# Kernel optimization log

Hardware: AMD Instinct MI355X
Metric: run time of the kernel (lower is better)

The kernel has to match this reference:

```python
import jax, jax.numpy as jnp
import numpy as np

T, N, F, H = 64, 20000, 8, 32
E = 320000
NEG_SLOPE = 0.01  # torch.nn.LeakyReLU default


def setup_inputs() -> dict:
    key = jax.random.key(0)
    ks = jax.random.split(key, 16)
    g = lambda k, shape, fan_in: jax.random.normal(k, shape, jnp.float32) * (1.0 / np.sqrt(fan_in))
    return {
        "x": jax.random.normal(ks[0], (T, N, F), jnp.float32),
        "edge_index": jax.random.randint(ks[1], (2, E), 0, N, jnp.int64),
        "edge_weight": jax.random.uniform(ks[2], (E,), jnp.float32),
        "h": jnp.zeros((N, H), jnp.float32),
        # GConvGRU(K=1): each ChebConv reduces to a dense Linear (only T_0 = X term)
        "Wxz": g(ks[3], (F, H), F), "bxz": jnp.zeros((H,), jnp.float32),
        "Whz": g(ks[4], (H, H), H), "bhz": jnp.zeros((H,), jnp.float32),
        "Wxr": g(ks[5], (F, H), F), "bxr": jnp.zeros((H,), jnp.float32),
        "Whr": g(ks[6], (H, H), H), "bhr": jnp.zeros((H,), jnp.float32),
        "Wxh": g(ks[7], (F, H), F), "bxh": jnp.zeros((H,), jnp.float32),
        "Whh": g(ks[8], (H, H), H), "bhh": jnp.zeros((H,), jnp.float32),
        "W1": g(ks[9], (H, 1), H), "b1": jnp.zeros((1,), jnp.float32),
        "W2": g(ks[10], (N, 1), N), "b2": jnp.zeros((1,), jnp.float32),
    }


def reference(x, edge_index, edge_weight, h,
              Wxz, bxz, Whz, bhz, Wxr, bxr, Whr, bhr, Wxh, bxh, Whh, bhh,
              W1, b1, W2, b2):
    # GConvGRU with Chebyshev order K=1: each ChebConv is out = X @ W + b
    # (edge_index / edge_weight only participate for K >= 2, faithful to source).
    def gru_step(hc, xt):  # hc: [N,H], xt: [N,F]
        z = jax.nn.sigmoid(xt @ Wxz + bxz + hc @ Whz + bhz)
        r = jax.nn.sigmoid(xt @ Wxr + bxr + hc @ Whr + bhr)
        h_tilde = jnp.tanh(xt @ Wxh + bxh + (hc * r) @ Whh + bhh)
        hn = z * hc + (1.0 - z) * h_tilde
        return hn, hn

    h_fin, h_tensor = jax.lax.scan(gru_step, h, x)  # h_tensor: [T,N,H]
    a = jax.nn.leaky_relu(h_tensor, NEG_SLOPE)       # LeakyReLU(h_tensor)
    a = jax.nn.leaky_relu(a @ W1 + b1, NEG_SLOPE)    # linear1 -> [T,N,1], then LeakyReLU
    a = a[..., 0]                                    # squeeze -> [T,N]
    out = (a @ W2 + b2)[..., 0]                      # linear2 -> [T,1] -> squeeze -> [T]
    return (out, h_fin)
```

## Files before the change

### kernel.cpp

```cpp
#include <hip/hip_runtime.h>
#include <hip/hip_bf16.h>

#define T_STEPS 64
#define N_NODES 20000
#define F_IN    8
#define H_DIM   32
#define NEG_SLOPE 0.01f
#define WS_STRIDE 32
#define LOG2E 1.44269504f

typedef __attribute__((ext_vector_type(8))) short bf16x8;
typedef __attribute__((ext_vector_type(4))) float f32x4;

#define MFMA(a, b, c) __builtin_amdgcn_mfma_f32_16x16x32_bf16((a), (b), (c), 0, 0, 0)

__device__ __forceinline__ unsigned short f2bf(float f) {
    unsigned u = __float_as_uint(f);
    u += 0x7FFFu + ((u >> 16) & 1u);
    return (unsigned short)(u >> 16);
}
__device__ __forceinline__ float bf2f(unsigned short s) {
    return __uint_as_float(((unsigned)s) << 16);
}
__device__ __forceinline__ void split_pack8_rne(const float* v, bf16x8& hi, bf16x8& lo) {
    union { unsigned u[4]; bf16x8 v8; } H, L;
#pragma unroll
    for (int p = 0; p < 4; ++p) {
        float a = v[2*p], b = v[2*p+1];
        unsigned short ha = f2bf(a), hb = f2bf(b);
        unsigned short la = f2bf(a - bf2f(ha)), lb = f2bf(b - bf2f(hb));
        H.u[p] = (unsigned)ha | ((unsigned)hb << 16);
        L.u[p] = (unsigned)la | ((unsigned)lb << 16);
    }
    hi = H.v8; lo = L.v8;
}

__device__ __forceinline__ unsigned cvtpk(float a, float b) {
    union { __hip_bfloat162 h; unsigned u; } U;
    U.h = __float22bfloat162_rn(float2{a, b});
    return U.u;
}


__device__ __forceinline__ void load_wfragW(const float* __restrict__ W, int c, int q,
                                            int Rout, int Rown, int Roth, float scale,
                                            bf16x8& hi, bf16x8& lo) {
    float v[8];
#pragma unroll
    for (int j = 0; j < 8; ++j) {
        int dim = (j < 4) ? (Rown + 4*q + j) : (Roth + 4*q + (j - 4));
        v[j] = W[dim * H_DIM + (Rout + c)] * scale;
    }
    split_pack8_rne(v, hi, lo);
}

__device__ __forceinline__ bf16x8 load_xwfragW(const float* __restrict__ Wx,
                                               const float* __restrict__ bx,
                                               const float* __restrict__ bh,
                                               int c, int q, int Rout, float scale) {
    union { unsigned short s[8]; bf16x8 v8; } U;
#pragma unroll
    for (int j = 0; j < 8; ++j) U.s[j] = 0;
    if (q == 0) {
#pragma unroll
        for (int j = 0; j < 8; ++j) U.s[j] = f2bf(Wx[j * H_DIM + Rout + c] * scale);
    } else if (q == 1) {
#pragma unroll
        for (int j = 0; j < 8; ++j) {
            float w0 = Wx[j * H_DIM + Rout + c] * scale;
            unsigned short h = f2bf(w0);
            U.s[j] = f2bf(w0 - bf2f(h));
        }
    } else if (q == 3) {
        float b = (bx[Rout + c] + bh[Rout + c]) * scale;
        unsigned short h = f2bf(b);
        U.s[0] = h;
        U.s[1] = f2bf(b - bf2f(h));
    }
    return U.v8;
}

__device__ __forceinline__ bf16x8 frag4(unsigned o01, unsigned o23,
                                        unsigned p01, unsigned p23) {
    union { unsigned u[4]; bf16x8 v8; } U;
    U.u[0] = o01; U.u[1] = o23; U.u[2] = p01; U.u[3] = p23;
    return U.v8;
}

__device__ __forceinline__ float sigmoid2_f(float xp) {
    return __builtin_amdgcn_rcpf(1.0f + __builtin_amdgcn_exp2f(-xp));
}
__device__ __forceinline__ float tanh2_f(float yp) {
    return 1.0f - 2.0f * __builtin_amdgcn_rcpf(1.0f + __builtin_amdgcn_exp2f(yp));
}
__device__ __forceinline__ float leaky_f(float x) {
    return fmaxf(x, NEG_SLOPE * x);
}

__global__ void final_kernel(const float* __restrict__ ws, const float* __restrict__ b2,
                             float* __restrict__ out) {
    int t = threadIdx.x;
    if (t < T_STEPS) out[t] = ws[t * WS_STRIDE] + b2[0];
}

__global__ __launch_bounds__(128, 3) void rgcn_mfma_kernel(
    const float* __restrict__ x,
    const float* __restrict__ h0,
    const float* __restrict__ Wxz, const float* __restrict__ bxz,
    const float* __restrict__ Whz, const float* __restrict__ bhz,
    const float* __restrict__ Wxr, const float* __restrict__ bxr,
    const float* __restrict__ Whr, const float* __restrict__ bhr,
    const float* __restrict__ Wxh, const float* __restrict__ bxh,
    const float* __restrict__ Whh, const float* __restrict__ bhh,
    const float* __restrict__ W1,  const float* __restrict__ b1,
    const float* __restrict__ W2,
    float* __restrict__ ws,
    float* __restrict__ out)
{
    const int tid  = threadIdx.x;
    const int w    = tid >> 6;
    const int l    = tid & 63;
    const int c    = l & 15;
    const int q    = l >> 4;
    const int base = blockIdx.x * 16;
    const int node = base + c;
    const int Rown = 16 * w;
    const int Roth = 16 - Rown;

    __shared__ __align__(16) unsigned xbuf[T_STEPS][16][4];
    __shared__ __align__(8) uint2 hxbuf[2][2][4][16];
    __shared__ __align__(8) uint2 rhbuf[2][4][16];
    __shared__ unsigned short pbuf16[T_STEPS][2][17];

    bf16x8 WHrh, WHrl, WHzh, WHzl, WHhh, WHhl;
    load_wfragW(Whr, c, q, Rown, Rown, Roth, LOG2E,        WHrh, WHrl);
    load_wfragW(Whz, c, q, Rown, Rown, Roth, LOG2E,        WHzh, WHzl);
    load_wfragW(Whh, c, q, Rown, Rown, Roth, 2.0f * LOG2E, WHhh, WHhl);
    bf16x8 WXr = load_xwfragW(Wxr, bxr, bhr, c, q, Rown, LOG2E);
    bf16x8 WXz = load_xwfragW(Wxz, bxz, bhz, c, q, Rown, LOG2E);
    bf16x8 WXh = load_xwfragW(Wxh, bxh, bhh, c, q, Rown, 2.0f * LOG2E);

    float w1v[4];
#pragma unroll
    for (int i = 0; i < 4; ++i) w1v[i] = W1[Rown + 4*q + i];
    const float b1s = b1[0];
    const float w2l = W2[node];

    float hv[4];
    unsigned own01, own23;
    {
        float4 h4 = ((const float4*)(h0 + (size_t)node * H_DIM + Rown))[q];
        hv[0] = h4.x; hv[1] = h4.y; hv[2] = h4.z; hv[3] = h4.w;
        own01 = cvtpk(hv[0], hv[1]);
        own23 = cvtpk(hv[2], hv[3]);
        hxbuf[0][w][q][c] = uint2{own01, own23};
    }

#pragma unroll
    for (int it = 0; it < 16; ++it) {
        int idx = it * 128 + tid;
        int t   = idx >> 5;
        int ce  = (idx >> 1) & 15;
        int hf  = idx & 1;
        const float4 v = *(const float4*)(
            x + ((size_t)t * N_NODES + base + ce) * F_IN + hf * 4);
        xbuf[t][ce][hf * 2]     = cvtpk(v.x, v.y);
        xbuf[t][ce][hf * 2 + 1] = cvtpk(v.z, v.w);
    }

    const f32x4 zero4 = {0.0f, 0.0f, 0.0f, 0.0f};
    const unsigned ONES2 = 0x3F803F80u;
    const bool q3 = (q == 3);

    __syncthreads();

    f32x4 axr, axz, axh;
    {
        union { uint4 u4; } X; X.u4 = *(const uint4*)&xbuf[0][c][0];
        bf16x8 fx0 = frag4(q3 ? ONES2 : X.u4.x, X.u4.y, X.u4.z, X.u4.w);
        axr = MFMA(WXr, fx0, zero4);
        axz = MFMA(WXz, fx0, zero4);
        axh = MFMA(WXh, fx0, zero4);
    }

#pragma unroll 1
    for (int t = 0; t < T_STEPS; ++t) {
        const int rp = t & 1;

        uint2 ohp = hxbuf[rp][1 - w][q][c];
        bf16x8 fh = frag4(own01, own23, ohp.x, ohp.y);

        f32x4 arA = MFMA(WHrh, fh, axr);
        f32x4 arB = MFMA(WHrl, fh, zero4);
        f32x4 az  = MFMA(WHzh, fh, axz);
        az        = MFMA(WHzl, fh, az);
        f32x4 ar  = arA + arB;

        float rh4[4];
#pragma unroll
        for (int i = 0; i < 4; ++i) rh4[i] = sigmoid2_f(ar[i]) * hv[i];
        unsigned rh01 = cvtpk(rh4[0], rh4[1]);
        unsigned rh23 = cvtpk(rh4[2], rh4[3]);
        rhbuf[w][q][c] = uint2{rh01, rh23};

        __syncthreads();

        int tt = (t + 1 < T_STEPS) ? (t + 1) : (T_STEPS - 1);
        union { uint4 u4; } X; X.u4 = *(const uint4*)&xbuf[tt][c][0];
        uint2 orh = rhbuf[1 - w][q][c];

        bf16x8 fxn = frag4(q3 ? ONES2 : X.u4.x, X.u4.y, X.u4.z, X.u4.w);
        f32x4 nxr = MFMA(WXr, fxn, zero4);
        f32x4 nxz = MFMA(WXz, fxn, zero4);
        f32x4 nxh = MFMA(WXh, fxn, zero4);

        float zv[4];
#pragma unroll
        for (int i = 0; i < 4; ++i) zv[i] = sigmoid2_f(az[i]);

        bf16x8 fr = frag4(rh01, rh23, orh.x, orh.y);
        f32x4 ahA = MFMA(WHhh, fr, axh);
        f32x4 ahB = MFMA(WHhl, fr, zero4);
        f32x4 ah  = ahA + ahB;

        float pnew = 0.0f;
#pragma unroll
        for (int i = 0; i < 4; ++i) {
            float th = tanh2_f(ah[i]);
            float hn = th + zv[i] * (hv[i] - th);
            hv[i] = hn;
            pnew = fmaf(leaky_f(hn), w1v[i], pnew);
        }
        pnew += __shfl_xor(pnew, 16);
        pnew += __shfl_xor(pnew, 32);
        if (l < 16) pbuf16[t][w][c] = (unsigned short)cvtpk(pnew, pnew);

        own01 = cvtpk(hv[0], hv[1]);
        own23 = cvtpk(hv[2], hv[3]);
        hxbuf[1 - rp][w][q][c] = uint2{own01, own23};

        axr = nxr; axz = nxz; axh = nxh;

        __syncthreads();
    }

#pragma unroll
    for (int rep = 0; rep < 8; ++rep) {
        int t = w * 32 + rep * 4 + q;
        float s = bf2f(pbuf16[t][0][c]) + bf2f(pbuf16[t][1][c]);
        float a2 = leaky_f(s + b1s) * w2l;
        a2 += __shfl_xor(a2, 1); a2 += __shfl_xor(a2, 2);
        a2 += __shfl_xor(a2, 4); a2 += __shfl_xor(a2, 8);
        if (c == 0) atomicAdd(&ws[t * WS_STRIDE], a2);
    }

    *(float4*)(out + T_STEPS + (size_t)node * H_DIM + Rown + 4*q) =
        (float4){hv[0], hv[1], hv[2], hv[3]};
}

extern "C" void kernel_launch(void* const* d_in, const int* in_sizes, int n_in,
                              void* d_out, int out_size, void* d_ws, size_t ws_size,
                              hipStream_t stream) {
    const float* x    = (const float*)d_in[0];
    const float* h0   = (const float*)d_in[3];
    const float* Wxz  = (const float*)d_in[4];
    const float* bxz  = (const float*)d_in[5];
    const float* Whz  = (const float*)d_in[6];
    const float* bhz  = (const float*)d_in[7];
    const float* Wxr  = (const float*)d_in[8];
    const float* bxr  = (const float*)d_in[9];
    const float* Whr  = (const float*)d_in[10];
    const float* bhr  = (const float*)d_in[11];
    const float* Wxh  = (const float*)d_in[12];
    const float* bxh  = (const float*)d_in[13];
    const float* Whh  = (const float*)d_in[14];
    const float* bhh  = (const float*)d_in[15];
    const float* W1   = (const float*)d_in[16];
    const float* b1   = (const float*)d_in[17];
    const float* W2   = (const float*)d_in[18];
    const float* b2   = (const float*)d_in[19];
    float* out = (float*)d_out;
    float* ws  = (float*)d_ws;

    const int grid = N_NODES / 16;
    rgcn_mfma_kernel<<<grid, 128, 0, stream>>>(
        x, h0, Wxz, bxz, Whz, bhz, Wxr, bxr, Whr, bhr,
        Wxh, bxh, Whh, bhh, W1, b1, W2, ws, out);

    final_kernel<<<1, 64, 0, stream>>>(ws, b2, out);
}
```

Measured before the change: 179.2 us.

## Compute reset gate redundantly for both halves to drop mid-step barrier

Each wave now also computes the reset gate for the other wave's half of the hidden state, using the other half's previous h already read from shared memory. It builds the full r*h fragment locally, so the rhbuf shared-memory exchange and one __syncthreads per timestep go away. In exchange each wave issues three extra MFMAs per step (two for the other half's Whr, one for its Wxr) and keeps more weight fragments in registers. The next-step x load is also hoisted to the top of the loop.

```diff
diff --git a/kernel.cpp b/kernel.cpp
--- a/kernel.cpp
+++ b/kernel.cpp
@@ -129,16 +129,17 @@
 
     __shared__ __align__(16) unsigned xbuf[T_STEPS][16][4];
     __shared__ __align__(8) uint2 hxbuf[2][2][4][16];
-    __shared__ __align__(8) uint2 rhbuf[2][4][16];
     __shared__ unsigned short pbuf16[T_STEPS][2][17];
 
-    bf16x8 WHrh, WHrl, WHzh, WHzl, WHhh, WHhl;
-    load_wfragW(Whr, c, q, Rown, Rown, Roth, LOG2E,        WHrh, WHrl);
-    load_wfragW(Whz, c, q, Rown, Rown, Roth, LOG2E,        WHzh, WHzl);
-    load_wfragW(Whh, c, q, Rown, Rown, Roth, 2.0f * LOG2E, WHhh, WHhl);
-    bf16x8 WXr = load_xwfragW(Wxr, bxr, bhr, c, q, Rown, LOG2E);
-    bf16x8 WXz = load_xwfragW(Wxz, bxz, bhz, c, q, Rown, LOG2E);
-    bf16x8 WXh = load_xwfragW(Wxh, bxh, bhh, c, q, Rown, 2.0f * LOG2E);
+    bf16x8 WHrOh, WHrOl, WHrTh, WHrTl, WHzh, WHzl, WHhh, WHhl;
+    load_wfragW(Whr, c, q, Rown, Rown, Roth, LOG2E,        WHrOh, WHrOl);
+    load_wfragW(Whr, c, q, Roth, Rown, Roth, LOG2E,        WHrTh, WHrTl);
+    load_wfragW(Whz, c, q, Rown, Rown, Roth, LOG2E,        WHzh,  WHzl);
+    load_wfragW(Whh, c, q, Rown, Rown, Roth, 2.0f * LOG2E, WHhh,  WHhl);
+    bf16x8 WXrO = load_xwfragW(Wxr, bxr, bhr, c, q, Rown, LOG2E);
+    bf16x8 WXrT = load_xwfragW(Wxr, bxr, bhr, c, q, Roth, LOG2E);
+    bf16x8 WXz  = load_xwfragW(Wxz, bxz, bhz, c, q, Rown, LOG2E);
+    bf16x8 WXh  = load_xwfragW(Wxh, bxh, bhh, c, q, Rown, 2.0f * LOG2E);
 
     float w1v[4];
 #pragma unroll
@@ -174,13 +175,14 @@
 
     __syncthreads();
 
-    f32x4 axr, axz, axh;
+    f32x4 axrO, axrT, axz, axh;
     {
-        union { uint4 u4; } X; X.u4 = *(const uint4*)&xbuf[0][c][0];
-        bf16x8 fx0 = frag4(q3 ? ONES2 : X.u4.x, X.u4.y, X.u4.z, X.u4.w);
-        axr = MFMA(WXr, fx0, zero4);
-        axz = MFMA(WXz, fx0, zero4);
-        axh = MFMA(WXh, fx0, zero4);
+        uint4 X = *(const uint4*)&xbuf[0][c][0];
+        bf16x8 fx0 = frag4(q3 ? ONES2 : X.x, X.y, X.z, X.w);
+        axrO = MFMA(WXrO, fx0, zero4);
+        axrT = MFMA(WXrT, fx0, zero4);
+        axz  = MFMA(WXz,  fx0, zero4);
+        axh  = MFMA(WXh,  fx0, zero4);
     }
 
 #pragma unroll 1
@@ -188,40 +190,49 @@
         const int rp = t & 1;
 
         uint2 ohp = hxbuf[rp][1 - w][q][c];
+        int tt = (t + 1 < T_STEPS) ? (t + 1) : (T_STEPS - 1);
+        uint4 X = *(const uint4*)&xbuf[tt][c][0];
+
         bf16x8 fh = frag4(own01, own23, ohp.x, ohp.y);
 
-        f32x4 arA = MFMA(WHrh, fh, axr);
-        f32x4 arB = MFMA(WHrl, fh, zero4);
-        f32x4 az  = MFMA(WHzh, fh, axz);
-        az        = MFMA(WHzl, fh, az);
-        f32x4 ar  = arA + arB;
-
-        float rh4[4];
-#pragma unroll
-        for (int i = 0; i < 4; ++i) rh4[i] = sigmoid2_f(ar[i]) * hv[i];
-        unsigned rh01 = cvtpk(rh4[0], rh4[1]);
-        unsigned rh23 = cvtpk(rh4[2], rh4[3]);
-        rhbuf[w][q][c] = uint2{rh01, rh23};
-
-        __syncthreads();
-
-        int tt = (t + 1 < T_STEPS) ? (t + 1) : (T_STEPS - 1);
-        union { uint4 u4; } X; X.u4 = *(const uint4*)&xbuf[tt][c][0];
-        uint2 orh = rhbuf[1 - w][q][c];
-
-        bf16x8 fxn = frag4(q3 ? ONES2 : X.u4.x, X.u4.y, X.u4.z, X.u4.w);
-        f32x4 nxr = MFMA(WXr, fxn, zero4);
-        f32x4 nxz = MFMA(WXz, fxn, zero4);
-        f32x4 nxh = MFMA(WXh, fxn, zero4);
+        f32x4 arOA = MFMA(WHrOh, fh, axrO);
+        f32x4 arOB = MFMA(WHrOl, fh, zero4);
+        f32x4 arTA = MFMA(WHrTh, fh, axrT);
+        f32x4 arTB = MFMA(WHrTl, fh, zero4);
+        f32x4 az   = MFMA(WHzh,  fh, axz);
+        az         = MFMA(WHzl,  fh, az);
+        f32x4 arO = arOA + arOB;
+        f32x4 arT = arTA + arTB;
+
+        float ph[4];
+        ph[0] = __uint_as_float(ohp.x << 16);
+        ph[1] = __uint_as_float(ohp.x & 0xffff0000u);
+        ph[2] = __uint_as_float(ohp.y << 16);
+        ph[3] = __uint_as_float(ohp.y & 0xffff0000u);
+
+        float rh8[8];
+#pragma unroll
+        for (int i = 0; i < 4; ++i) {
+            rh8[i]     = sigmoid2_f(arO[i]) * hv[i];
+            rh8[4 + i] = sigmoid2_f(arT[i]) * ph[i];
+        }
+        bf16x8 frh = frag4(cvtpk(rh8[0], rh8[1]), cvtpk(rh8[2], rh8[3]),
+                           cvtpk(rh8[4], rh8[5]), cvtpk(rh8[6], rh8[7]));
+
+        f32x4 ahA = MFMA(WHhh, frh, axh);
+        f32x4 ahB = MFMA(WHhl, frh, zero4);
+
+        bf16x8 fxn = frag4(q3 ? ONES2 : X.x, X.y, X.z, X.w);
+        f32x4 nxrO = MFMA(WXrO, fxn, zero4);
+        f32x4 nxrT = MFMA(WXrT, fxn, zero4);
+        f32x4 nxz  = MFMA(WXz,  fxn, zero4);
+        f32x4 nxh  = MFMA(WXh,  fxn, zero4);
 
         float zv[4];
 #pragma unroll
         for (int i = 0; i < 4; ++i) zv[i] = sigmoid2_f(az[i]);
 
-        bf16x8 fr = frag4(rh01, rh23, orh.x, orh.y);
-        f32x4 ahA = MFMA(WHhh, fr, axh);
-        f32x4 ahB = MFMA(WHhl, fr, zero4);
-        f32x4 ah  = ahA + ahB;
+        f32x4 ah = ahA + ahB;
 
         float pnew = 0.0f;
 #pragma unroll
@@ -239,7 +250,7 @@
         own23 = cvtpk(hv[2], hv[3]);
         hxbuf[1 - rp][w][q][c] = uint2{own01, own23};
 
-        axr = nxr; axz = nxz; axh = nxh;
+        axrO = nxrO; axrT = nxrT; axz = nxz; axh = nxh;
 
         __syncthreads();
     }
```

After: 191.6 us. 6.9% more time.
